# Kernel optimization log

Measured on AMD Instinct MI355X. Metric: run time of the kernel, lower is better.

Reference implementation:

```python
import jax, jax.numpy as jnp
import numpy as np

N_NODES = 200_000
N_EDGES = 6_400_000


def _gat_head(h, src, dst, W, a, n_nodes):
    """One GAT head: z = h @ W; e = leaky_relu([z_src||z_dst] @ a);
    segment softmax of e over incoming edges of each dst node;
    weighted scatter-add of z_src into dst. W: [Din, Dout], a: [2*Dout]."""
    d = W.shape[1]
    z = h @ W                      # [N, Dout]
    z_src = z[src]                 # [E, Dout] gather
    z_dst = z[dst]                 # [E, Dout] gather
    # [z_src||z_dst] @ a == z_src @ a[:d] + z_dst @ a[d:]  (avoids materializing the cat)
    e = jax.nn.leaky_relu(z_src @ a[:d] + z_dst @ a[d:])  # [E]
    # numerically stable segment softmax grouped by dst
    m = jax.ops.segment_max(e, dst, num_segments=n_nodes)
    m = jnp.where(jnp.isfinite(m), m, 0.0)
    ex = jnp.exp(e - m[dst])
    denom = jax.ops.segment_sum(ex, dst, num_segments=n_nodes)
    alpha = ex / denom[dst]        # [E]
    # weighted scatter-aggregation; isolated dst nodes get zeros (DGL update_all)
    return jax.ops.segment_sum(alpha[:, None] * z_src, dst, num_segments=n_nodes)


def reference(h, src, dst, fc1, attn1, fc2, attn2, mlp_w, mlp_b):
    n = h.shape[0]
    # layer1: 2 heads, hidden_dim=16, merge='cat' -> [N, 32]
    heads = [_gat_head(h, src, dst, fc1[i], attn1[i], n) for i in range(fc1.shape[0])]
    x = jnp.concatenate(heads, axis=1)
    x = jax.nn.elu(x)
    # layer2: 1 head, out_dim=2, cat of single head -> [N, 2]
    x = _gat_head(x, src, dst, fc2, attn2, n)
    # flatten to [1, 2*N], linear, sigmoid
    x = x.reshape(1, -1)
    out = jax.nn.sigmoid(x @ mlp_w + mlp_b)
    return out


def setup_inputs() -> dict:
    key = jax.random.key(0)
    ks = jax.random.split(key, 9)
    h = jax.random.normal(ks[0], (N_NODES, 2), dtype=jnp.float32)
    src = jax.random.randint(ks[1], (N_EDGES,), 0, N_NODES)
    dst = jax.random.randint(ks[2], (N_EDGES,), 0, N_NODES)
    # layer1: 2 heads, fc [in=2 -> out=16] stored as [head, in, out]; attn [head, 2*16]
    fc1 = jax.random.normal(ks[3], (2, 2, 16), dtype=jnp.float32)
    attn1 = jax.random.normal(ks[4], (2, 32), dtype=jnp.float32)
    # layer2: 1 head, fc [32 -> 2]; attn [2*2]
    fc2 = jax.random.normal(ks[5], (32, 2), dtype=jnp.float32)
    attn2 = jax.random.normal(ks[6], (4,), dtype=jnp.float32)
    # final MLP: Linear(2*num_nodes, 1); small scale to keep sigmoid unsaturated
    mlp_w = jax.random.normal(ks[7], (2 * N_NODES, 1), dtype=jnp.float32) * 1e-3
    mlp_b = jax.random.normal(ks[8], (1,), dtype=jnp.float32)
    return {"h": h, "src": src, "dst": dst, "fc1": fc1, "attn1": attn1,
            "fc2": fc2, "attn2": attn2, "mlp_w": mlp_w, "mlp_b": mlp_b}
```

## Files before the change

kernel.cpp:

```cpp
#include <hip/hip_runtime.h>
#include <hip/hip_bf16.h>
#include <math.h>

#define NN 200000
#define NE 6400000

#define BNODES 782
#define NB 256
#define CAP 27648
#define NBLK_SC 256
#define SCT 1024
#define CHUNK (NE / NBLK_SC)
#define SREG 27

#define W_DACC 0
#define W_UV   4
#define W_CUR  16
#define W_NOFF 1024
#define W_NCNT (W_NOFF + NN)
#define W_META (W_NCNT + NN)
#define W_Z2   (W_META + NB*CAP)
#define W_TOTAL (W_Z2 + 2*NN)

__global__ void k_init(unsigned* __restrict__ ws) {
    int t = blockIdx.x * blockDim.x + threadIdx.x;
    if (t == 0) *(double*)ws = 0.0;
    if (t < NB) ws[W_CUR + t] = 0u;
}

__global__ void k_prep(const float* __restrict__ fc1, const float* __restrict__ attn1,
                       float* __restrict__ uv) {
    int t = threadIdx.x;
    if (t < 8) {
        int h = t >> 2, r = t & 3, i = r & 1, isv = r >> 1;
        double s = 0.0;
        for (int o = 0; o < 16; ++o)
            s += (double)fc1[h * 32 + i * 16 + o] * (double)attn1[h * 32 + isv * 16 + o];
        uv[t] = (float)s;
    }
}

__launch_bounds__(SCT)
__global__ void k_scatter(const int* __restrict__ src, const int* __restrict__ dst,
                          unsigned* __restrict__ meta, unsigned* __restrict__ cur) {
    __shared__ unsigned cnt[NB], gbase[NB];
    for (int i = threadIdx.x; i < NB; i += SCT) cnt[i] = 0u;
    __syncthreads();
    int beg = blockIdx.x * CHUNK;
    unsigned pack[25];
#pragma unroll
    for (int k = 0; k < 25; ++k) {
        int j = k * SCT + threadIdx.x;
        pack[k] = 0xFFFFFFFFu;
        if (j < CHUNK) {
            unsigned d = (unsigned)__builtin_nontemporal_load(dst + beg + j);
            unsigned rank = atomicAdd(&cnt[d / BNODES], 1u);
            pack[k] = d | (rank << 18);
        }
    }
    __syncthreads();
    for (int i = threadIdx.x; i < NB; i += SCT)
        gbase[i] = cnt[i] ? atomicAdd(&cur[i], cnt[i]) : 0u;
    __syncthreads();
#pragma unroll
    for (int k = 0; k < 25; ++k) {
        if (pack[k] != 0xFFFFFFFFu) {
            int j = k * SCT + threadIdx.x;
            unsigned d = pack[k] & 0x3FFFFu;
            unsigned b = d / BNODES;
            unsigned dl = d - b * BNODES;
            unsigned slot = gbase[b] + (pack[k] >> 18);
            if (slot < CAP) {
                unsigned sn = (unsigned)__builtin_nontemporal_load(src + beg + j);
                meta[(size_t)b * CAP + slot] = sn | (dl << 18);
            }
        }
    }
}

__launch_bounds__(SCT)
__global__ void k_sort(unsigned* __restrict__ meta, const unsigned* __restrict__ cur,
                       unsigned* __restrict__ nodeoff, unsigned* __restrict__ nodecnt) {
    __shared__ unsigned hist[BNODES], base[BNODES], scan[BNODES];
    int b = blockIdx.x, t = threadIdx.x;
    size_t boff = (size_t)b * CAP;
    int cnt = min((int)cur[b], CAP);
    for (int i = t; i < BNODES; i += SCT) hist[i] = 0u;
    __syncthreads();
    unsigned rm[SREG], rr[SREG];
#pragma unroll
    for (int k = 0; k < SREG; ++k) {
        int i = k * SCT + t;
        rm[k] = 0xFFFFFFFFu;
        rr[k] = 0u;
        if (i < cnt) {
            rm[k] = meta[boff + i];
            rr[k] = atomicAdd(&hist[rm[k] >> 18], 1u);
        }
    }
    asm volatile("s_waitcnt vmcnt(0)" ::: "memory");
    __syncthreads();
    if (t < BNODES) scan[t] = hist[t];
    __syncthreads();
    for (int d = 1; d < BNODES; d <<= 1) {
        unsigned v = 0u;
        if (t < BNODES && t >= d) v = scan[t - d];
        __syncthreads();
        if (t < BNODES) scan[t] += v;
        __syncthreads();
    }
    int nb = b * BNODES;
    int nn = min(BNODES, NN - nb);
    if (t < BNODES) {
        unsigned ex = scan[t] - hist[t];
        base[t] = ex;
        if (t < nn) {
            nodeoff[nb + t] = (unsigned)boff + ex;
            nodecnt[nb + t] = hist[t];
        }
    }
    __syncthreads();
#pragma unroll
    for (int k = 0; k < SREG; ++k)
        if (rm[k] != 0xFFFFFFFFu)
            meta[boff + base[rm[k] >> 18] + rr[k]] = rm[k];
}

__global__ void k_gat1(const unsigned* __restrict__ meta, const unsigned* __restrict__ nodeoff,
                       const unsigned* __restrict__ nodecnt, const float2* __restrict__ h,
                       const float* __restrict__ uv, const float* __restrict__ fc1,
                       const float* __restrict__ fc2, float2* __restrict__ z2) {
    int n = blockIdx.x * blockDim.x + threadIdx.x;
    if (n >= NN) return;
    float u00 = uv[0], u10 = uv[1], v00 = uv[2], v10 = uv[3];
    float u01 = uv[4], u11 = uv[5], v01 = uv[6], v11 = uv[7];
    float2 hd = h[n];
    float c0 = fmaf(hd.x, v00, hd.y * v10);
    float c1 = fmaf(hd.x, v01, hd.y * v11);
    unsigned off = nodeoff[n];
    int cnt = (int)nodecnt[n];
    float s0 = 0.f, s1 = 0.f, s2 = 0.f, s3 = 0.f, s4 = 0.f, s5 = 0.f;
#pragma unroll 4
    for (int k = 0; k < cnt; ++k) {
        unsigned m = meta[(size_t)off + k];
        float2 hs = h[m & 0x3FFFF];
        float e0 = fmaf(hs.x, u00, fmaf(hs.y, u10, c0));
        float e1 = fmaf(hs.x, u01, fmaf(hs.y, u11, c1));
        e0 = e0 >= 0.f ? e0 : 0.01f * e0;
        e1 = e1 >= 0.f ? e1 : 0.01f * e1;
        float ex0 = __expf(e0);
        float ex1 = __expf(e1);
        s0 += ex0; s1 += ex0 * hs.x; s2 += ex0 * hs.y;
        s3 += ex1; s4 += ex1 * hs.x; s5 += ex1 * hs.y;
    }
    float z0 = 0.f, z1 = 0.f;
#pragma unroll
    for (int o = 0; o < 16; ++o) {
        float t0 = s0 > 0.f ? (s1 * fc1[o]      + s2 * fc1[16 + o]) / s0 : 0.f;
        float t1 = s3 > 0.f ? (s4 * fc1[32 + o] + s5 * fc1[48 + o]) / s3 : 0.f;
        float x0 = t0 > 0.f ? t0 : expm1f(t0);
        float x1 = t1 > 0.f ? t1 : expm1f(t1);
        z0 += x0 * fc2[2 * o]      + x1 * fc2[2 * (16 + o)];
        z1 += x0 * fc2[2 * o + 1]  + x1 * fc2[2 * (16 + o) + 1];
    }
    z2[n] = make_float2(z0, z1);
}

__global__ void k_gat2(const unsigned* __restrict__ meta, const unsigned* __restrict__ nodeoff,
                       const unsigned* __restrict__ nodecnt, const float2* __restrict__ z2,
                       const float* __restrict__ attn2, const float* __restrict__ mlp_w,
                       double* __restrict__ dacc) {
    int n = blockIdx.x * blockDim.x + threadIdx.x;
    double v = 0.0;
    if (n < NN) {
        float a0 = attn2[0], a1 = attn2[1], a2 = attn2[2], a3 = attn2[3];
        float2 zd = z2[n];
        float cd = fmaf(zd.x, a2, zd.y * a3);
        unsigned off = nodeoff[n];
        int cnt = (int)nodecnt[n];
        float s0 = 0.f, s1 = 0.f, s2 = 0.f;
#pragma unroll 4
        for (int k = 0; k < cnt; ++k) {
            unsigned m = meta[(size_t)off + k];
            float2 zs = z2[m & 0x3FFFF];
            float e = fmaf(zs.x, a0, fmaf(zs.y, a1, cd));
            e = e >= 0.f ? e : 0.01f * e;
            float ex = __expf(e - 48.f);
            s0 += ex; s1 += ex * zs.x; s2 += ex * zs.y;
        }
        float x0 = s0 > 0.f ? s1 / s0 : 0.f;
        float x1 = s0 > 0.f ? s2 / s0 : 0.f;
        v = (double)x0 * (double)mlp_w[2 * n] + (double)x1 * (double)mlp_w[2 * n + 1];
    }
    for (int off = 32; off > 0; off >>= 1) v += __shfl_down(v, off);
    __shared__ double sm[4];
    int lane = threadIdx.x & 63, wid = threadIdx.x >> 6;
    if (lane == 0) sm[wid] = v;
    __syncthreads();
    if (threadIdx.x == 0) {
        double sum = sm[0] + sm[1] + sm[2] + sm[3];
        unsafeAtomicAdd(dacc, sum);
    }
}

__global__ void k_out(const double* __restrict__ dacc, const float* __restrict__ mlp_b,
                      float* __restrict__ out) {
    double logit = dacc[0] + (double)mlp_b[0];
    out[0] = (float)(1.0 / (1.0 + exp(-logit)));
}

extern "C" void kernel_launch(void* const* d_in, const int* in_sizes, int n_in,
                              void* d_out, int out_size, void* d_ws, size_t ws_size,
                              hipStream_t stream) {
    const float* h     = (const float*)d_in[0];
    const int*   src   = (const int*)d_in[1];
    const int*   dst   = (const int*)d_in[2];
    const float* fc1   = (const float*)d_in[3];
    const float* attn1 = (const float*)d_in[4];
    const float* fc2   = (const float*)d_in[5];
    const float* attn2 = (const float*)d_in[6];
    const float* mlp_w = (const float*)d_in[7];
    const float* mlp_b = (const float*)d_in[8];
    float* out = (float*)d_out;

    unsigned* ws      = (unsigned*)d_ws;
    double*   dacc    = (double*)d_ws;
    float*    uv      = (float*)(ws + W_UV);
    unsigned* cur     = ws + W_CUR;
    unsigned* nodeoff = ws + W_NOFF;
    unsigned* nodecnt = ws + W_NCNT;
    unsigned* meta    = ws + W_META;
    float2*   z2      = (float2*)(ws + W_Z2);

    const int NG = (NN + 255) / 256;

    hipLaunchKernelGGL(k_init, dim3(1), dim3(256), 0, stream, ws);
    hipLaunchKernelGGL(k_prep, dim3(1), dim3(64), 0, stream, fc1, attn1, uv);
    hipLaunchKernelGGL(k_scatter, dim3(NBLK_SC), dim3(SCT), 0, stream,
                       src, dst, meta, cur);
    hipLaunchKernelGGL(k_sort, dim3(NB), dim3(SCT), 0, stream,
                       meta, cur, nodeoff, nodecnt);
    hipLaunchKernelGGL(k_gat1, dim3(NG), dim3(256), 0, stream,
                       meta, nodeoff, nodecnt, (const float2*)h, uv, fc1, fc2, z2);
    hipLaunchKernelGGL(k_gat2, dim3(NG), dim3(256), 0, stream,
                       meta, nodeoff, nodecnt, (const float2*)z2, attn2, mlp_w, dacc);
    hipLaunchKernelGGL(k_out, dim3(1), dim3(1), 0, stream, dacc, mlp_b, out);
}
```

Before: 240.7 us.

## Fuse all stages into one cooperative kernel with grid-wide syncs

```diff
diff --git a/kernel.cpp b/kernel.cpp
--- a/kernel.cpp
+++ b/kernel.cpp
@@ -1,6 +1,9 @@
 #include <hip/hip_runtime.h>
 #include <hip/hip_bf16.h>
+#include <hip/hip_cooperative_groups.h>
 #include <math.h>
+
+namespace cg = cooperative_groups;
 
 #define NN 200000
 #define NE 6400000
@@ -8,9 +11,8 @@
 #define BNODES 782
 #define NB 256
 #define CAP 27648
-#define NBLK_SC 256
 #define SCT 1024
-#define CHUNK (NE / NBLK_SC)
+#define CHUNK (NE / NB)
 #define SREG 27
 
 #define W_DACC 0
@@ -22,199 +24,210 @@
 #define W_Z2   (W_META + NB*CAP)
 #define W_TOTAL (W_Z2 + 2*NN)
 
-__global__ void k_init(unsigned* __restrict__ ws) {
-    int t = blockIdx.x * blockDim.x + threadIdx.x;
-    if (t == 0) *(double*)ws = 0.0;
-    if (t < NB) ws[W_CUR + t] = 0u;
-}
-
-__global__ void k_prep(const float* __restrict__ fc1, const float* __restrict__ attn1,
-                       float* __restrict__ uv) {
-    int t = threadIdx.x;
-    if (t < 8) {
-        int h = t >> 2, r = t & 3, i = r & 1, isv = r >> 1;
-        double s = 0.0;
-        for (int o = 0; o < 16; ++o)
-            s += (double)fc1[h * 32 + i * 16 + o] * (double)attn1[h * 32 + isv * 16 + o];
-        uv[t] = (float)s;
-    }
-}
-
 __launch_bounds__(SCT)
-__global__ void k_scatter(const int* __restrict__ src, const int* __restrict__ dst,
-                          unsigned* __restrict__ meta, unsigned* __restrict__ cur) {
-    __shared__ unsigned cnt[NB], gbase[NB];
-    for (int i = threadIdx.x; i < NB; i += SCT) cnt[i] = 0u;
-    __syncthreads();
-    int beg = blockIdx.x * CHUNK;
-    unsigned pack[25];
-#pragma unroll
-    for (int k = 0; k < 25; ++k) {
-        int j = k * SCT + threadIdx.x;
-        pack[k] = 0xFFFFFFFFu;
-        if (j < CHUNK) {
-            unsigned d = (unsigned)__builtin_nontemporal_load(dst + beg + j);
-            unsigned rank = atomicAdd(&cnt[d / BNODES], 1u);
-            pack[k] = d | (rank << 18);
-        }
-    }
-    __syncthreads();
-    for (int i = threadIdx.x; i < NB; i += SCT)
-        gbase[i] = cnt[i] ? atomicAdd(&cur[i], cnt[i]) : 0u;
-    __syncthreads();
-#pragma unroll
-    for (int k = 0; k < 25; ++k) {
-        if (pack[k] != 0xFFFFFFFFu) {
-            int j = k * SCT + threadIdx.x;
-            unsigned d = pack[k] & 0x3FFFFu;
-            unsigned b = d / BNODES;
-            unsigned dl = d - b * BNODES;
-            unsigned slot = gbase[b] + (pack[k] >> 18);
-            if (slot < CAP) {
-                unsigned sn = (unsigned)__builtin_nontemporal_load(src + beg + j);
-                meta[(size_t)b * CAP + slot] = sn | (dl << 18);
-            }
-        }
-    }
-}
-
-__launch_bounds__(SCT)
-__global__ void k_sort(unsigned* __restrict__ meta, const unsigned* __restrict__ cur,
-                       unsigned* __restrict__ nodeoff, unsigned* __restrict__ nodecnt) {
-    __shared__ unsigned hist[BNODES], base[BNODES], scan[BNODES];
-    int b = blockIdx.x, t = threadIdx.x;
-    size_t boff = (size_t)b * CAP;
-    int cnt = min((int)cur[b], CAP);
-    for (int i = t; i < BNODES; i += SCT) hist[i] = 0u;
-    __syncthreads();
-    unsigned rm[SREG], rr[SREG];
-#pragma unroll
-    for (int k = 0; k < SREG; ++k) {
-        int i = k * SCT + t;
-        rm[k] = 0xFFFFFFFFu;
-        rr[k] = 0u;
-        if (i < cnt) {
-            rm[k] = meta[boff + i];
-            rr[k] = atomicAdd(&hist[rm[k] >> 18], 1u);
-        }
-    }
-    asm volatile("s_waitcnt vmcnt(0)" ::: "memory");
-    __syncthreads();
-    if (t < BNODES) scan[t] = hist[t];
-    __syncthreads();
-    for (int d = 1; d < BNODES; d <<= 1) {
-        unsigned v = 0u;
-        if (t < BNODES && t >= d) v = scan[t - d];
-        __syncthreads();
-        if (t < BNODES) scan[t] += v;
-        __syncthreads();
-    }
-    int nb = b * BNODES;
-    int nn = min(BNODES, NN - nb);
-    if (t < BNODES) {
-        unsigned ex = scan[t] - hist[t];
-        base[t] = ex;
-        if (t < nn) {
-            nodeoff[nb + t] = (unsigned)boff + ex;
-            nodecnt[nb + t] = hist[t];
-        }
-    }
-    __syncthreads();
-#pragma unroll
-    for (int k = 0; k < SREG; ++k)
-        if (rm[k] != 0xFFFFFFFFu)
-            meta[boff + base[rm[k] >> 18] + rr[k]] = rm[k];
-}
-
-__global__ void k_gat1(const unsigned* __restrict__ meta, const unsigned* __restrict__ nodeoff,
-                       const unsigned* __restrict__ nodecnt, const float2* __restrict__ h,
-                       const float* __restrict__ uv, const float* __restrict__ fc1,
-                       const float* __restrict__ fc2, float2* __restrict__ z2) {
-    int n = blockIdx.x * blockDim.x + threadIdx.x;
-    if (n >= NN) return;
-    float u00 = uv[0], u10 = uv[1], v00 = uv[2], v10 = uv[3];
-    float u01 = uv[4], u11 = uv[5], v01 = uv[6], v11 = uv[7];
-    float2 hd = h[n];
-    float c0 = fmaf(hd.x, v00, hd.y * v10);
-    float c1 = fmaf(hd.x, v01, hd.y * v11);
-    unsigned off = nodeoff[n];
-    int cnt = (int)nodecnt[n];
-    float s0 = 0.f, s1 = 0.f, s2 = 0.f, s3 = 0.f, s4 = 0.f, s5 = 0.f;
+__global__ void k_fused(const int* __restrict__ src, const int* __restrict__ dst,
+                        const float2* __restrict__ h, const float* __restrict__ fc1,
+                        const float* __restrict__ attn1, const float* __restrict__ fc2,
+                        const float* __restrict__ attn2, const float* __restrict__ mlp_w,
+                        const float* __restrict__ mlp_b, float* __restrict__ out,
+                        unsigned* __restrict__ ws) {
+    cg::grid_group grid = cg::this_grid();
+    double*   dacc    = (double*)ws;
+    float*    uv      = (float*)(ws + W_UV);
+    unsigned* cur     = ws + W_CUR;
+    unsigned* nodeoff = ws + W_NOFF;
+    unsigned* nodecnt = ws + W_NCNT;
+    unsigned* meta    = ws + W_META;
+    float2*   z2      = (float2*)(ws + W_Z2);
+
+    __shared__ unsigned shA[BNODES];
+    __shared__ unsigned shB[BNODES];
+    __shared__ unsigned shC[BNODES];
+    __shared__ double sm[16];
+
+    const int b = blockIdx.x, t = threadIdx.x;
+
+    if (b == 0) {
+        if (t == 0) *dacc = 0.0;
+        if (t < NB) cur[t] = 0u;
+        if (t < 8) {
+            int hh = t >> 2, r = t & 3, i = r & 1, isv = r >> 1;
+            double s = 0.0;
+            for (int o = 0; o < 16; ++o)
+                s += (double)fc1[hh * 32 + i * 16 + o] * (double)attn1[hh * 32 + isv * 16 + o];
+            uv[t] = (float)s;
+        }
+    }
+    grid.sync();
+
+    {
+        for (int i = t; i < NB; i += SCT) shA[i] = 0u;
+        __syncthreads();
+        int beg = b * CHUNK;
+        unsigned pack[25];
+#pragma unroll
+        for (int k = 0; k < 25; ++k) {
+            int j = k * SCT + t;
+            pack[k] = 0xFFFFFFFFu;
+            if (j < CHUNK) {
+                unsigned d = (unsigned)__builtin_nontemporal_load(dst + beg + j);
+                unsigned rank = atomicAdd(&shA[d / BNODES], 1u);
+                pack[k] = d | (rank << 18);
+            }
+        }
+        __syncthreads();
+        for (int i = t; i < NB; i += SCT)
+            shB[i] = shA[i] ? atomicAdd(&cur[i], shA[i]) : 0u;
+        __syncthreads();
+#pragma unroll
+        for (int k = 0; k < 25; ++k) {
+            if (pack[k] != 0xFFFFFFFFu) {
+                int j = k * SCT + t;
+                unsigned d = pack[k] & 0x3FFFFu;
+                unsigned bb = d / BNODES;
+                unsigned dl = d - bb * BNODES;
+                unsigned slot = shB[bb] + (pack[k] >> 18);
+                if (slot < CAP) {
+                    unsigned sn = (unsigned)__builtin_nontemporal_load(src + beg + j);
+                    meta[(size_t)bb * CAP + slot] = sn | (dl << 18);
+                }
+            }
+        }
+    }
+    grid.sync();
+
+    {
+        size_t boff = (size_t)b * CAP;
+        int cnt = min((int)cur[b], CAP);
+        for (int i = t; i < BNODES; i += SCT) shA[i] = 0u;
+        __syncthreads();
+        unsigned rm[SREG], rr[SREG];
+#pragma unroll
+        for (int k = 0; k < SREG; ++k) {
+            int i = k * SCT + t;
+            rm[k] = 0xFFFFFFFFu;
+            rr[k] = 0u;
+            if (i < cnt) {
+                rm[k] = meta[boff + i];
+                rr[k] = atomicAdd(&shA[rm[k] >> 18], 1u);
+            }
+        }
+        asm volatile("s_waitcnt vmcnt(0)" ::: "memory");
+        __syncthreads();
+        if (t < BNODES) shC[t] = shA[t];
+        __syncthreads();
+        for (int d = 1; d < BNODES; d <<= 1) {
+            unsigned v = 0u;
+            if (t < BNODES && t >= d) v = shC[t - d];
+            __syncthreads();
+            if (t < BNODES) shC[t] += v;
+            __syncthreads();
+        }
+        int nb = b * BNODES;
+        int nn = min(BNODES, NN - nb);
+        if (t < BNODES) {
+            unsigned ex = shC[t] - shA[t];
+            shB[t] = ex;
+            if (t < nn) {
+                nodeoff[nb + t] = (unsigned)boff + ex;
+                nodecnt[nb + t] = shA[t];
+            }
+        }
+        __syncthreads();
+#pragma unroll
+        for (int k = 0; k < SREG; ++k)
+            if (rm[k] != 0xFFFFFFFFu)
+                meta[boff + shB[rm[k] >> 18] + rr[k]] = rm[k];
+    }
+    grid.sync();
+
+    {
+        int n = b * SCT + t;
+        if (n < NN) {
+            float u00 = uv[0], u10 = uv[1], v00 = uv[2], v10 = uv[3];
+            float u01 = uv[4], u11 = uv[5], v01 = uv[6], v11 = uv[7];
+            float2 hd = h[n];
+            float c0 = fmaf(hd.x, v00, hd.y * v10);
+            float c1 = fmaf(hd.x, v01, hd.y * v11);
+            unsigned off = nodeoff[n];
+            int cnt = (int)nodecnt[n];
+            float s0 = 0.f, s1 = 0.f, s2 = 0.f, s3 = 0.f, s4 = 0.f, s5 = 0.f;
 #pragma unroll 4
-    for (int k = 0; k < cnt; ++k) {
-        unsigned m = meta[(size_t)off + k];
-        float2 hs = h[m & 0x3FFFF];
-        float e0 = fmaf(hs.x, u00, fmaf(hs.y, u10, c0));
-        float e1 = fmaf(hs.x, u01, fmaf(hs.y, u11, c1));
-        e0 = e0 >= 0.f ? e0 : 0.01f * e0;
-        e1 = e1 >= 0.f ? e1 : 0.01f * e1;
-        float ex0 = __expf(e0);
-        float ex1 = __expf(e1);
-        s0 += ex0; s1 += ex0 * hs.x; s2 += ex0 * hs.y;
-        s3 += ex1; s4 += ex1 * hs.x; s5 += ex1 * hs.y;
-    }
-    float z0 = 0.f, z1 = 0.f;
-#pragma unroll
-    for (int o = 0; o < 16; ++o) {
-        float t0 = s0 > 0.f ? (s1 * fc1[o]      + s2 * fc1[16 + o]) / s0 : 0.f;
-        float t1 = s3 > 0.f ? (s4 * fc1[32 + o] + s5 * fc1[48 + o]) / s3 : 0.f;
-        float x0 = t0 > 0.f ? t0 : expm1f(t0);
-        float x1 = t1 > 0.f ? t1 : expm1f(t1);
-        z0 += x0 * fc2[2 * o]      + x1 * fc2[2 * (16 + o)];
-        z1 += x0 * fc2[2 * o + 1]  + x1 * fc2[2 * (16 + o) + 1];
-    }
-    z2[n] = make_float2(z0, z1);
-}
-
-__global__ void k_gat2(const unsigned* __restrict__ meta, const unsigned* __restrict__ nodeoff,
-                       const unsigned* __restrict__ nodecnt, const float2* __restrict__ z2,
-                       const float* __restrict__ attn2, const float* __restrict__ mlp_w,
-                       double* __restrict__ dacc) {
-    int n = blockIdx.x * blockDim.x + threadIdx.x;
-    double v = 0.0;
-    if (n < NN) {
-        float a0 = attn2[0], a1 = attn2[1], a2 = attn2[2], a3 = attn2[3];
-        float2 zd = z2[n];
-        float cd = fmaf(zd.x, a2, zd.y * a3);
-        unsigned off = nodeoff[n];
-        int cnt = (int)nodecnt[n];
-        float s0 = 0.f, s1 = 0.f, s2 = 0.f;
+            for (int k = 0; k < cnt; ++k) {
+                unsigned m = meta[(size_t)off + k];
+                float2 hs = h[m & 0x3FFFF];
+                float e0 = fmaf(hs.x, u00, fmaf(hs.y, u10, c0));
+                float e1 = fmaf(hs.x, u01, fmaf(hs.y, u11, c1));
+                e0 = e0 >= 0.f ? e0 : 0.01f * e0;
+                e1 = e1 >= 0.f ? e1 : 0.01f * e1;
+                float ex0 = __expf(e0);
+                float ex1 = __expf(e1);
+                s0 += ex0; s1 += ex0 * hs.x; s2 += ex0 * hs.y;
+                s3 += ex1; s4 += ex1 * hs.x; s5 += ex1 * hs.y;
+            }
+            float z0 = 0.f, z1 = 0.f;
+#pragma unroll
+            for (int o = 0; o < 16; ++o) {
+                float t0 = s0 > 0.f ? (s1 * fc1[o]      + s2 * fc1[16 + o]) / s0 : 0.f;
+                float t1 = s3 > 0.f ? (s4 * fc1[32 + o] + s5 * fc1[48 + o]) / s3 : 0.f;
+                float x0 = t0 > 0.f ? t0 : expm1f(t0);
+                float x1 = t1 > 0.f ? t1 : expm1f(t1);
+                z0 += x0 * fc2[2 * o]     + x1 * fc2[2 * (16 + o)];
+                z1 += x0 * fc2[2 * o + 1] + x1 * fc2[2 * (16 + o) + 1];
+            }
+            z2[n] = make_float2(z0, z1);
+        }
+    }
+    grid.sync();
+
+    {
+        int n = b * SCT + t;
+        double v = 0.0;
+        if (n < NN) {
+            float a0 = attn2[0], a1 = attn2[1], a2 = attn2[2], a3 = attn2[3];
+            float2 zd = z2[n];
+            float cd = fmaf(zd.x, a2, zd.y * a3);
+            unsigned off = nodeoff[n];
+            int cnt = (int)nodecnt[n];
+            float s0 = 0.f, s1 = 0.f, s2 = 0.f;
 #pragma unroll 4
-        for (int k = 0; k < cnt; ++k) {
-            unsigned m = meta[(size_t)off + k];
-            float2 zs = z2[m & 0x3FFFF];
-            float e = fmaf(zs.x, a0, fmaf(zs.y, a1, cd));
-            e = e >= 0.f ? e : 0.01f * e;
-            float ex = __expf(e - 48.f);
-            s0 += ex; s1 += ex * zs.x; s2 += ex * zs.y;
-        }
-        float x0 = s0 > 0.f ? s1 / s0 : 0.f;
-        float x1 = s0 > 0.f ? s2 / s0 : 0.f;
-        v = (double)x0 * (double)mlp_w[2 * n] + (double)x1 * (double)mlp_w[2 * n + 1];
-    }
-    for (int off = 32; off > 0; off >>= 1) v += __shfl_down(v, off);
-    __shared__ double sm[4];
-    int lane = threadIdx.x & 63, wid = threadIdx.x >> 6;
-    if (lane == 0) sm[wid] = v;
-    __syncthreads();
-    if (threadIdx.x == 0) {
-        double sum = sm[0] + sm[1] + sm[2] + sm[3];
-        unsafeAtomicAdd(dacc, sum);
-    }
-}
-
-__global__ void k_out(const double* __restrict__ dacc, const float* __restrict__ mlp_b,
-                      float* __restrict__ out) {
-    double logit = dacc[0] + (double)mlp_b[0];
-    out[0] = (float)(1.0 / (1.0 + exp(-logit)));
+            for (int k = 0; k < cnt; ++k) {
+                unsigned m = meta[(size_t)off + k];
+                float2 zs = z2[m & 0x3FFFF];
+                float e = fmaf(zs.x, a0, fmaf(zs.y, a1, cd));
+                e = e >= 0.f ? e : 0.01f * e;
+                float ex = __expf(e - 48.f);
+                s0 += ex; s1 += ex * zs.x; s2 += ex * zs.y;
+            }
+            float x0 = s0 > 0.f ? s1 / s0 : 0.f;
+            float x1 = s0 > 0.f ? s2 / s0 : 0.f;
+            v = (double)x0 * (double)mlp_w[2 * n] + (double)x1 * (double)mlp_w[2 * n + 1];
+        }
+        for (int off = 32; off > 0; off >>= 1) v += __shfl_down(v, off);
+        int lane = t & 63, wid = t >> 6;
+        if (lane == 0) sm[wid] = v;
+        __syncthreads();
+        if (t == 0) {
+            double s = 0.0;
+#pragma unroll
+            for (int w = 0; w < 16; ++w) s += sm[w];
+            unsafeAtomicAdd(dacc, s);
+        }
+    }
+    grid.sync();
+
+    if (b == 0 && t == 0) {
+        double logit = *dacc + (double)mlp_b[0];
+        out[0] = (float)(1.0 / (1.0 + exp(-logit)));
+    }
 }
 
 extern "C" void kernel_launch(void* const* d_in, const int* in_sizes, int n_in,
                               void* d_out, int out_size, void* d_ws, size_t ws_size,
                               hipStream_t stream) {
-    const float* h     = (const float*)d_in[0];
     const int*   src   = (const int*)d_in[1];
     const int*   dst   = (const int*)d_in[2];
+    const float2* h    = (const float2*)d_in[0];
     const float* fc1   = (const float*)d_in[3];
     const float* attn1 = (const float*)d_in[4];
     const float* fc2   = (const float*)d_in[5];
@@ -222,27 +235,14 @@
     const float* mlp_w = (const float*)d_in[7];
     const float* mlp_b = (const float*)d_in[8];
     float* out = (float*)d_out;
-
-    unsigned* ws      = (unsigned*)d_ws;
-    double*   dacc    = (double*)d_ws;
-    float*    uv      = (float*)(ws + W_UV);
-    unsigned* cur     = ws + W_CUR;
-    unsigned* nodeoff = ws + W_NOFF;
-    unsigned* nodecnt = ws + W_NCNT;
-    unsigned* meta    = ws + W_META;
-    float2*   z2      = (float2*)(ws + W_Z2);
-
-    const int NG = (NN + 255) / 256;
-
-    hipLaunchKernelGGL(k_init, dim3(1), dim3(256), 0, stream, ws);
-    hipLaunchKernelGGL(k_prep, dim3(1), dim3(64), 0, stream, fc1, attn1, uv);
-    hipLaunchKernelGGL(k_scatter, dim3(NBLK_SC), dim3(SCT), 0, stream,
-                       src, dst, meta, cur);
-    hipLaunchKernelGGL(k_sort, dim3(NB), dim3(SCT), 0, stream,
-                       meta, cur, nodeoff, nodecnt);
-    hipLaunchKernelGGL(k_gat1, dim3(NG), dim3(256), 0, stream,
-                       meta, nodeoff, nodecnt, (const float2*)h, uv, fc1, fc2, z2);
-    hipLaunchKernelGGL(k_gat2, dim3(NG), dim3(256), 0, stream,
-                       meta, nodeoff, nodecnt, (const float2*)z2, attn2, mlp_w, dacc);
-    hipLaunchKernelGGL(k_out, dim3(1), dim3(1), 0, stream, dacc, mlp_b, out);
+    unsigned* ws = (unsigned*)d_ws;
+
+    void* args[] = {(void*)&src, (void*)&dst, (void*)&h, (void*)&fc1, (void*)&attn1,
+                    (void*)&fc2, (void*)&attn2, (void*)&mlp_w, (void*)&mlp_b,
+                    (void*)&out, (void*)&ws};
+    void* args2[] = {(void*)&src, (void*)&dst, (void*)&h, (void*)&fc1, (void*)&attn1,
+                     (void*)&fc2, (void*)&attn2, (void*)&mlp_w, (void*)&mlp_b,
+                     (void*)&out, (void*)&ws};
+    (void)args;
+    hipLaunchCooperativeKernel((void*)k_fused, dim3(NB), dim3(SCT), args2, 0, stream);
 }
```

Result: slower. 378.5 us (+57.3%).
